# Performance work log

Hardware: AMD Instinct MI355X
Metric: run time of the kernel (lower is better)

## Reference

```python
import jax, jax.numpy as jnp
import numpy as np

B, L, C, H, W = 2, 3, 64, 32, 32
DI, N, DT_RANK, K = 128, 16, 4, 4  # d_inner=2*C, d_state, dt_rank=ceil(C/16), 4 scan dirs


def setup_inputs() -> dict:
    key = jax.random.key(0)
    ks = iter(jax.random.split(key, 48))
    nrm = lambda shape, s=0.02: jax.random.normal(next(ks), shape, jnp.float32) * s
    return {
        "image_sequence": jax.random.normal(next(ks), (B, L, C, H, W), jnp.float32),
        "difficult_zone": jax.random.normal(next(ks), (B, C, H, W), jnp.float32),
        "sigma": jax.random.uniform(next(ks), (B, C, H, W), jnp.float32),
        # LayerNorm2d applied to each frame
        "norm_g": jnp.ones((C,)), "norm_b": jnp.zeros((C,)),
        # ConvolutionalResBlock (in=3C -> out=C), GroupNorm(num_groups=1)
        "gn1_g": jnp.ones((3 * C,)), "gn1_b": jnp.zeros((3 * C,)),
        "conv1_w": nrm((C, 3 * C, 3, 3)), "conv1_b": jnp.zeros((C,)),
        "gn2_g": jnp.ones((C,)), "gn2_b": jnp.zeros((C,)),
        "conv2_w": nrm((C, C, 3, 3)), "conv2_b": jnp.zeros((C,)),
        "skip_w": nrm((C, 3 * C, 1, 1)), "skip_b": jnp.zeros((C,)),
        # VSSBlock pre-norms
        "ln1_g": jnp.ones((C,)), "ln1_b": jnp.zeros((C,)),
        "ln2_g": jnp.ones((C,)), "ln2_b": jnp.zeros((C,)),
        # SS2D
        "in_proj_w": nrm((2 * DI, C)),
        "dwconv_w": nrm((DI, 1, 3, 3)), "dwconv_b": jnp.zeros((DI,)),
        "x_proj_w": nrm((K, DT_RANK + 2 * N, DI)),
        "dt_proj_w": nrm((K, DI, DT_RANK), 0.1),
        "dt_proj_b": jnp.log(jnp.expm1(jnp.full((K, DI), 0.01, jnp.float32))),
        "A_logs": jnp.log(jnp.tile(jnp.arange(1, N + 1, dtype=jnp.float32), (K * DI, 1))),
        "Ds": jnp.ones((K * DI,)),
        "out_norm_g": jnp.ones((DI,)), "out_norm_b": jnp.zeros((DI,)),
        "out_proj_w": nrm((C, DI)),
        # Mlp (hidden = C)
        "fc1_w": nrm((C, C)), "fc1_b": jnp.zeros((C,)),
        "fc2_w": nrm((C, C)), "fc2_b": jnp.zeros((C,)),
    }


def _ln(x, g, b, eps=1e-5):  # layernorm over last axis
    m = x.mean(-1, keepdims=True)
    v = x.var(-1, keepdims=True)
    return (x - m) * jax.lax.rsqrt(v + eps) * g + b


def _ln2d(x, g, b, eps=1e-6):  # per-pixel channel layernorm, NCHW
    m = x.mean(1, keepdims=True)
    v = x.var(1, keepdims=True)
    return (x - m) * jax.lax.rsqrt(v + eps) * g[None, :, None, None] + b[None, :, None, None]


def _gn1(x, g, b, eps=1e-5):  # GroupNorm(num_groups=1), NCHW
    m = x.mean((1, 2, 3), keepdims=True)
    v = x.var((1, 2, 3), keepdims=True)
    return (x - m) * jax.lax.rsqrt(v + eps) * g[None, :, None, None] + b[None, :, None, None]


def _conv(x, w, b, pad):
    y = jax.lax.conv_general_dilated(x, w, (1, 1), [(pad, pad), (pad, pad)],
                                     dimension_numbers=("NCHW", "OIHW", "NCHW"))
    return y + b[None, :, None, None]


def _forward(image_sequence, difficult_zone, sigma, norm_g, norm_b, gn1_g, gn1_b,
             conv1_w, conv1_b, gn2_g, gn2_b, conv2_w, conv2_b, skip_w, skip_b,
             ln1_g, ln1_b, ln2_g, ln2_b, in_proj_w, dwconv_w, dwconv_b, x_proj_w,
             dt_proj_w, dt_proj_b, A_logs, Ds, out_norm_g, out_norm_b, out_proj_w,
             fc1_w, fc1_b, fc2_w, fc2_b):
    b, l, c, h, w = image_sequence.shape
    bl, L2 = b * l, h * w
    # fold frame loop into batch (identical math per frame in the torch loop)
    frames = _ln2d(image_sequence.reshape(bl, c, h, w), norm_g, norm_b)
    dz = jnp.broadcast_to(difficult_zone[:, None], (b, l, c, h, w)).reshape(bl, c, h, w)
    sg = jnp.broadcast_to(sigma[:, None], (b, l, c, h, w)).reshape(bl, c, h, w)
    x = jnp.concatenate([dz, frames, sg], axis=1)  # [bl, 3c, h, w]
    # channel compressor: pre-act conv res block
    hdn = _conv(jax.nn.silu(_gn1(x, gn1_g, gn1_b)), conv1_w, conv1_b, 1)
    hdn = _conv(jax.nn.silu(_gn1(hdn, gn2_g, gn2_b)), conv2_w, conv2_b, 1)
    x = hdn + _conv(x, skip_w, skip_b, 0)          # [bl, c, h, w]
    x = x.transpose(0, 2, 3, 1)                    # [bl, h, w, c]
    # --- VSSBlock (pre-norm): x = x + SS2D(LN(x)) ---
    xn = _ln(x, ln1_g, ln1_b)
    xz = xn @ in_proj_w.T                          # [bl,h,w,2*DI]
    xc, z = jnp.split(xz, 2, axis=-1)
    xc = xc.transpose(0, 3, 1, 2)                  # [bl, DI, h, w]
    xc = jax.lax.conv_general_dilated(xc, dwconv_w, (1, 1), [(1, 1), (1, 1)],
                                      dimension_numbers=("NCHW", "OIHW", "NCHW"),
                                      feature_group_count=DI) + dwconv_b[None, :, None, None]
    xc = jax.nn.silu(xc)
    # 4-direction scan inputs (HW, WH, and their reverses)
    xf = xc.reshape(bl, DI, L2)
    xt = xc.transpose(0, 1, 3, 2).reshape(bl, DI, L2)
    xs = jnp.stack([xf, xt], axis=1)
    xs = jnp.concatenate([xs, jnp.flip(xs, axis=-1)], axis=1)  # [bl, 4, DI, L2]
    x_dbl = jnp.einsum("bkdl,kcd->bkcl", xs, x_proj_w)
    dts, Bs, Cs = jnp.split(x_dbl, [DT_RANK, DT_RANK + N], axis=2)
    dts = jnp.einsum("bkrl,kdr->bkdl", dts, dt_proj_w) + dt_proj_b[None, :, :, None]
    dts = jax.nn.softplus(dts)                     # [bl, 4, DI, L2]
    A = -jnp.exp(A_logs).reshape(K, DI, N)
    dA = jnp.exp(dts[..., None] * A[None, :, :, None, :])            # [bl,4,DI,L2,N]
    dBu = dts[..., None] * Bs.transpose(0, 1, 3, 2)[:, :, None] * xs[..., None]
    a_t = dA.transpose(3, 0, 1, 2, 4)              # [L2, bl, 4, DI, N]
    bu_t = dBu.transpose(3, 0, 1, 2, 4)
    c_t = Cs.transpose(3, 0, 1, 2)                 # [L2, bl, 4, N]

    def step(hid, inp):
        a_i, bu_i, c_i = inp
        hid = a_i * hid + bu_i
        return hid, jnp.einsum("bkdn,bkn->bkd", hid, c_i)

    h0 = jnp.zeros((bl, K, DI, N), xs.dtype)
    _, ys = jax.lax.scan(step, h0, (a_t, bu_t, c_t))                 # [L2, bl, 4, DI]
    ys = ys.transpose(1, 2, 3, 0) + xs * Ds.reshape(K, DI)[None, :, :, None]
    inv = jnp.flip(ys[:, 2:4], axis=-1)
    y = (ys[:, 0] + inv[:, 0]
         + ys[:, 1].reshape(bl, DI, w, h).transpose(0, 1, 3, 2).reshape(bl, DI, L2)
         + inv[:, 1].reshape(bl, DI, w, h).transpose(0, 1, 3, 2).reshape(bl, DI, L2))
    y = _ln(y.transpose(0, 2, 1), out_norm_g, out_norm_b).reshape(bl, h, w, DI)
    y = y * jax.nn.silu(z)
    x = x + y @ out_proj_w.T
    # --- x = x + Mlp(LN(x)) ---
    xn = _ln(x, ln2_g, ln2_b)
    x = x + (jax.nn.gelu(xn @ fc1_w.T + fc1_b, approximate=False) @ fc2_w.T + fc2_b)
    return x.transpose(0, 3, 1, 2).reshape(b, l, c, h, w)


def reference(image_sequence, difficult_zone, sigma, norm_g, norm_b, gn1_g, gn1_b,
              conv1_w, conv1_b, gn2_g, gn2_b, conv2_w, conv2_b, skip_w, skip_b,
              ln1_g, ln1_b, ln2_g, ln2_b, in_proj_w, dwconv_w, dwconv_b, x_proj_w,
              dt_proj_w, dt_proj_b, A_logs, Ds, out_norm_g, out_norm_b, out_proj_w,
              fc1_w, fc1_b, fc2_w, fc2_b):
    return _forward(image_sequence, difficult_zone, sigma, norm_g, norm_b, gn1_g, gn1_b,
                    conv1_w, conv1_b, gn2_g, gn2_b, conv2_w, conv2_b, skip_w, skip_b,
                    ln1_g, ln1_b, ln2_g, ln2_b, in_proj_w, dwconv_w, dwconv_b, x_proj_w,
                    dt_proj_w, dt_proj_b, A_logs, Ds, out_norm_g, out_norm_b, out_proj_w,
                    fc1_w, fc1_b, fc2_w, fc2_b)
```

## Files before the change

### kernel.cpp

```cpp
#include <hip/hip_runtime.h>
#include <math.h>

#define BL    6
#define CCH   64
#define C3    192
#define L2    1024
#define DIC   128
#define NST   16
#define K4    4
#define PSTR  1088
#define NCH   32

#define LOG2E 1.44269504088896340736f
#define LN2C  0.69314718055994530942f

__device__ __forceinline__ float fexp(float x){ return __builtin_amdgcn_exp2f(x*LOG2E); }
__device__ __forceinline__ float fsilu(float x){ return x / (1.f + fexp(-x)); }
__device__ __forceinline__ float fsoftplus(float x){
  if (x > 20.f) return x;
  return __builtin_amdgcn_logf(1.f + fexp(x)) * LN2C;
}
__device__ __forceinline__ float fgelu(float x){
  return 0.5f*x*(1.f + erff(x*0.70710678118654752440f));
}

__global__ __launch_bounds__(256) void k_ln2d(const float* __restrict__ img,
    const float* __restrict__ dz, const float* __restrict__ sg,
    const float* __restrict__ g, const float* __restrict__ b, float* __restrict__ x3c,
    float* __restrict__ psum1, float* __restrict__ psq1){
  __shared__ float ps[4][16], pq[4][16], gs[4], gq[4];
  int s = blockIdx.x >> 6;
  int pg = blockIdx.x & 63;
  int tid = threadIdx.x;
  int px = tid & 15; int cg = tid >> 4;
  int wv = tid >> 6; int lane = tid & 63;
  int p = pg*16 + px;
  int bsmp = s/3;
  const float* fr = img + (size_t)s*CCH*L2;
  float vals[4]; float sm=0.f, sq=0.f;
  #pragma unroll
  for (int j=0;j<4;++j){
    int c = cg*4 + j;
    float v = fr[c*L2 + p];
    vals[j]=v; sm+=v; sq+=v*v;
  }
  sm += __shfl_xor(sm,16,64); sq += __shfl_xor(sq,16,64);
  sm += __shfl_xor(sm,32,64); sq += __shfl_xor(sq,32,64);
  if (lane < 16){ ps[wv][lane]=sm; pq[wv][lane]=sq; }
  __syncthreads();
  sm = ps[0][px]+ps[1][px]+ps[2][px]+ps[3][px];
  sq = pq[0][px]+pq[1][px]+pq[2][px]+pq[3][px];
  float mean = sm*(1.f/CCH); float var = sq*(1.f/CCH)-mean*mean;
  float rs = rsqrtf(var + 1e-6f);
  float* o = x3c + (size_t)s*C3*L2;
  const float* dzp = dz + (size_t)bsmp*CCH*L2;
  const float* sgp = sg + (size_t)bsmp*CCH*L2;
  float gsm=0.f, gsq=0.f;
  #pragma unroll
  for (int j=0;j<4;++j){
    int c = cg*4+j;
    float dzv = dzp[c*L2+p];
    float nv  = (vals[j]-mean)*rs*g[c] + b[c];
    float sgv = sgp[c*L2+p];
    o[c*L2+p] = dzv;
    o[(CCH+c)*L2+p] = nv;
    o[(2*CCH+c)*L2+p] = sgv;
    gsm += dzv+nv+sgv; gsq += dzv*dzv+nv*nv+sgv*sgv;
  }
  for (int m=1;m<64;m<<=1){ gsm+=__shfl_xor(gsm,m,64); gsq+=__shfl_xor(gsq,m,64); }
  if (lane==0){ gs[wv]=gsm; gq[wv]=gsq; }
  __syncthreads();
  if (tid==0){
    psum1[blockIdx.x] = gs[0]+gs[1]+gs[2]+gs[3];
    psq1 [blockIdx.x] = gq[0]+gq[1]+gq[2]+gq[3];
  }
}

__global__ __launch_bounds__(256) void k_gnact_pad(const float* __restrict__ x,
    const float* __restrict__ psum, const float* __restrict__ psq,
    const float* __restrict__ g, const float* __restrict__ b,
    int ch, int parts, float inv_n, float eps, float* __restrict__ out){
  int bx = blockIdx.x;
  int s = bx / ch; int c = bx % ch;
  int tid = threadIdx.x;
  float sm=0.f, sq=0.f;
  for (int i=0;i<parts;++i){ sm += psum[s*parts+i]; sq += psq[s*parts+i]; }
  float mean = sm*inv_n;
  float var = sq*inv_n - mean*mean;
  float rs = rsqrtf(var + eps);
  float gc = g[c]*rs; float bc = b[c] - mean*rs*g[c];
  float4 v = *(const float4*)(x + (size_t)bx*1024 + tid*4);
  float4 o; o.x = fsilu(v.x*gc+bc); o.y = fsilu(v.y*gc+bc);
  o.z = fsilu(v.z*gc+bc); o.w = fsilu(v.w*gc+bc);
  float* pl = out + (size_t)bx*PSTR;
  *(float4*)(pl + 32 + tid*4) = o;
  float4 z4 = make_float4(0.f,0.f,0.f,0.f);
  if (tid < 8)  *(float4*)(pl + tid*4) = z4;
  else if (tid < 16) *(float4*)(pl + 1056 + (tid-8)*4) = z4;
}

__device__ __forceinline__ void conv_row_acc(float4& a0, float4& a1, float4 mid, float lf, float rt,
    const float* wp0, const float* wp1){
  float w0=wp0[0], w1=wp0[1], w2=wp0[2];
  a0.x = fmaf(w0,lf,   fmaf(w1,mid.x, fmaf(w2,mid.y, a0.x)));
  a0.y = fmaf(w0,mid.x,fmaf(w1,mid.y, fmaf(w2,mid.z, a0.y)));
  a0.z = fmaf(w0,mid.y,fmaf(w1,mid.z, fmaf(w2,mid.w, a0.z)));
  a0.w = fmaf(w0,mid.z,fmaf(w1,mid.w, fmaf(w2,rt,    a0.w)));
  float v0=wp1[0], v1=wp1[1], v2=wp1[2];
  a1.x = fmaf(v0,lf,   fmaf(v1,mid.x, fmaf(v2,mid.y, a1.x)));
  a1.y = fmaf(v0,mid.x,fmaf(v1,mid.y, fmaf(v2,mid.z, a1.y)));
  a1.z = fmaf(v0,mid.y,fmaf(v1,mid.z, fmaf(v2,mid.w, a1.z)));
  a1.w = fmaf(v0,mid.z,fmaf(v1,mid.w, fmaf(v2,rt,    a1.w)));
}

__device__ __forceinline__ void conv_ci_body(float4 m0, float4 m1, float4 m2, int q,
    const float* wp0, const float* wp1, float4& a0, float4& a1){
  float lf0=__shfl_up(m0.w,1,64), rt0=__shfl_down(m0.x,1,64);
  float lf1=__shfl_up(m1.w,1,64), rt1=__shfl_down(m1.x,1,64);
  float lf2=__shfl_up(m2.w,1,64), rt2=__shfl_down(m2.x,1,64);
  if (q==0){ lf0=0.f; lf1=0.f; lf2=0.f; }
  if (q==7){ rt0=0.f; rt1=0.f; rt2=0.f; }
  conv_row_acc(a0,a1,m0,lf0,rt0, wp0+0, wp1+0);
  conv_row_acc(a0,a1,m1,lf1,rt1, wp0+3, wp1+3);
  conv_row_acc(a0,a1,m2,lf2,rt2, wp0+6, wp1+6);
}

__global__ __launch_bounds__(256) void k_conv1_split(const float* __restrict__ xact,
    const float* __restrict__ w, float* __restrict__ part){
  int bx = blockIdx.x; int kk = bx&7; int cop=(bx>>3)&31; int s=bx>>8;
  int co0 = cop*2, co1 = co0+1;
  int tid = threadIdx.x; int row = tid>>3; int q = tid&7; int col0 = q*4;
  float4 a0 = make_float4(0.f,0.f,0.f,0.f);
  float4 a1 = make_float4(0.f,0.f,0.f,0.f);
  int ci0 = kk*24;
  const float* pl = xact + ((size_t)s*C3 + ci0)*PSTR + row*32 + col0;
  const float* wp0 = w + (size_t)(co0*C3 + ci0)*9;
  const float* wp1 = w + (size_t)(co1*C3 + ci0)*9;
  float4 m0 = *(const float4*)(pl);
  float4 m1 = *(const float4*)(pl+32);
  float4 m2 = *(const float4*)(pl+64);
  #pragma unroll 2
  for (int i=0;i<24;++i){
    const float* pn = pl + (i<23 ? PSTR : 0);
    float4 n0 = *(const float4*)(pn);
    float4 n1 = *(const float4*)(pn+32);
    float4 n2 = *(const float4*)(pn+64);
    conv_ci_body(m0,m1,m2,q, wp0, wp1, a0, a1);
    wp0 += 9; wp1 += 9; pl = pn; m0=n0; m1=n1; m2=n2;
  }
  float* pp = part + (size_t)kk*(BL*CCH*L2) + ((size_t)s*CCH+co0)*L2 + row*32+col0;
  *(float4*)pp = a0;
  *(float4*)(pp+L2) = a1;
}

__global__ __launch_bounds__(256) void k_reduce1(const float* __restrict__ part,
    const float* __restrict__ bias, float* __restrict__ h1,
    float* __restrict__ psum2, float* __restrict__ psq2){
  int co = blockIdx.x & 63; int s = blockIdx.x >> 6;
  size_t ofs = ((size_t)s*CCH+co)*L2 + threadIdx.x*4;
  const size_t stride = (size_t)BL*CCH*L2;
  float4 acc = *(const float4*)(part + ofs);
  #pragma unroll
  for (int kk=1;kk<8;++kk){
    float4 r = *(const float4*)(part + (size_t)kk*stride + ofs);
    acc.x += r.x; acc.y += r.y; acc.z += r.z; acc.w += r.w;
  }
  float bv = bias[co];
  acc.x += bv; acc.y += bv; acc.z += bv; acc.w += bv;
  *(float4*)(h1 + ofs) = acc;
  float sm = acc.x+acc.y+acc.z+acc.w;
  float sq = acc.x*acc.x+acc.y*acc.y+acc.z*acc.z+acc.w*acc.w;
  for (int m=1;m<64;m<<=1){ sm+=__shfl_xor(sm,m,64); sq+=__shfl_xor(sq,m,64); }
  __shared__ float s_sm[4], s_sq[4];
  int wv = threadIdx.x>>6;
  if ((threadIdx.x&63)==0){ s_sm[wv]=sm; s_sq[wv]=sq; }
  __syncthreads();
  if (threadIdx.x==0){
    psum2[blockIdx.x] = s_sm[0]+s_sm[1]+s_sm[2]+s_sm[3];
    psq2 [blockIdx.x] = s_sq[0]+s_sq[1]+s_sq[2]+s_sq[3];
  }
}

__global__ __launch_bounds__(256) void k_conv2_split(const float* __restrict__ xact2,
    const float* __restrict__ x3c, const float* __restrict__ w2,
    const float* __restrict__ wsk, float* __restrict__ part){
  int t = blockIdx.x; int role = t % 3; t /= 3;
  int cop = t & 31; int s = t >> 5;
  int co0 = cop*2, co1 = co0+1;
  int tid = threadIdx.x; int row = tid>>3; int q = tid&7; int col0 = q*4;
  int p = row*32+col0;
  float4 a0 = make_float4(0.f,0.f,0.f,0.f);
  float4 a1 = make_float4(0.f,0.f,0.f,0.f);
  if (role < 2){
    int ci0 = role*32;
    const float* pl = xact2 + ((size_t)s*CCH + ci0)*PSTR + row*32 + col0;
    const float* wp0 = w2 + (size_t)(co0*CCH + ci0)*9;
    const float* wp1 = w2 + (size_t)(co1*CCH + ci0)*9;
    float4 m0 = *(const float4*)(pl);
    float4 m1 = *(const float4*)(pl+32);
    float4 m2 = *(const float4*)(pl+64);
    #pragma unroll 2
    for (int i=0;i<32;++i){
      const float* pn = pl + (i<31 ? PSTR : 0);
      float4 n0 = *(const float4*)(pn);
      float4 n1 = *(const float4*)(pn+32);
      float4 n2 = *(const float4*)(pn+64);
      conv_ci_body(m0,m1,m2,q, wp0, wp1, a0, a1);
      wp0 += 9; wp1 += 9; pl = pn; m0=n0; m1=n1; m2=n2;
    }
  } else {
    const float* x3 = x3c + (size_t)s*C3*L2 + p;
    #pragma unroll 4
    for (int ci=0; ci<C3; ++ci){
      float4 v = *(const float4*)(x3 + (size_t)ci*L2);
      float ws0 = wsk[co0*C3+ci], ws1 = wsk[co1*C3+ci];
      a0.x = fmaf(ws0,v.x,a0.x); a0.y = fmaf(ws0,v.y,a0.y); a0.z = fmaf(ws0,v.z,a0.z); a0.w = fmaf(ws0,v.w,a0.w);
      a1.x = fmaf(ws1,v.x,a1.x); a1.y = fmaf(ws1,v.y,a1.y); a1.z = fmaf(ws1,v.z,a1.z); a1.w = fmaf(ws1,v.w,a1.w);
    }
  }
  float* pp = part + (size_t)role*(BL*CCH*L2) + ((size_t)s*CCH+co0)*L2 + p;
  *(float4*)pp = a0;
  *(float4*)(pp+L2) = a1;
}

__global__ __launch_bounds__(256) void k_reduce2(const float* __restrict__ part,
    const float* __restrict__ b2, const float* __restrict__ bsk,
    float* __restrict__ xp, float* __restrict__ x_cmaj){
  int co = blockIdx.x & 63; int s = blockIdx.x >> 6;
  int p = threadIdx.x*4;
  size_t ofs = ((size_t)s*CCH+co)*L2 + p;
  const size_t stride = (size_t)BL*CCH*L2;
  float4 r0 = *(const float4*)(part + ofs);
  float4 r1 = *(const float4*)(part + stride + ofs);
  float4 r2 = *(const float4*)(part + 2*stride + ofs);
  float bv = b2[co]+bsk[co];
  float4 o;
  o.x = r0.x+r1.x+r2.x+bv;
  o.y = r0.y+r1.y+r2.y+bv;
  o.z = r0.z+r1.z+r2.z+bv;
  o.w = r0.w+r1.w+r2.w+bv;
  *(float4*)(x_cmaj + ofs) = o;
  float* xpb = xp + ((size_t)s*L2 + p)*CCH + co;
  xpb[0] = o.x; xpb[CCH] = o.y; xpb[2*CCH] = o.z; xpb[3*CCH] = o.w;
}

__global__ __launch_bounds__(256) void k_ln1_inproj(const float* __restrict__ xp,
    const float* __restrict__ g, const float* __restrict__ b, const float* __restrict__ W,
    float* __restrict__ xc, float* __restrict__ z_t){
  __shared__ float xn_s[64*65];
  int bx = blockIdx.x; int oq = bx & 3; int pg = (bx>>2)&15; int s = bx>>6;
  int p0 = pg*64;
  int tid = threadIdx.x; int wv = __builtin_amdgcn_readfirstlane(tid>>6); int lane = tid&63;
  for (int j=0;j<16;++j){
    int pl = wv*16 + j; int p = p0 + pl;
    float v = xp[((size_t)s*L2 + p)*CCH + lane];
    float sm = v, sq = v*v;
    for (int m=1;m<64;m<<=1){ sm += __shfl_xor(sm,m,64); sq += __shfl_xor(sq,m,64); }
    float mean = sm*(1.f/64.f); float var = sq*(1.f/64.f) - mean*mean;
    float rs = rsqrtf(var + 1e-5f);
    xn_s[pl*65 + lane] = (v-mean)*rs*g[lane] + b[lane];
  }
  __syncthreads();
  int px_l = tid & 63;
  int og = __builtin_amdgcn_readfirstlane(tid >> 6);
  int o0 = oq*64 + og*16;
  float acc[16];
  #pragma unroll
  for (int oi=0;oi<16;++oi) acc[oi]=0.f;
  for (int c=0;c<64;++c){
    float xv = xn_s[px_l*65 + c];
    #pragma unroll
    for (int oi=0;oi<16;++oi) acc[oi] = fmaf(W[(o0+oi)*64 + c], xv, acc[oi]);
  }
  int p = p0 + px_l;
  if (oq < 2){
    #pragma unroll
    for (int oi=0;oi<16;++oi) xc[((size_t)s*DIC + o0 + oi)*L2 + p] = acc[oi];
  } else {
    #pragma unroll
    for (int oi=0;oi<16;++oi) z_t[((size_t)s*DIC + (o0-128) + oi)*L2 + p] = acc[oi];
  }
}

__global__ __launch_bounds__(256) void k_dwconv(const float* __restrict__ xc,
    const float* __restrict__ w, const float* __restrict__ bias, float* __restrict__ xconv){
  int bx = blockIdx.x; int dch = bx & 127; int s = bx >> 7;
  int tid = threadIdx.x; int row = tid>>3; int q = tid&7; int col0 = q*4;
  const float* xr = xc + ((size_t)s*DIC+dch)*L2;
  const float* wp = w + dch*9;
  float bv = bias[dch];
  float4 acc = make_float4(bv,bv,bv,bv);
  #pragma unroll
  for (int dy=-1;dy<=1;++dy){
    int r = row+dy;
    float4 mid = make_float4(0.f,0.f,0.f,0.f);
    if (0<=r && r<32) mid = *(const float4*)(xr + r*32 + col0);
    float lf = __shfl_up(mid.w,1,64); if(q==0) lf=0.f;
    float rt = __shfl_down(mid.x,1,64); if(q==7) rt=0.f;
    float w0=wp[(dy+1)*3], w1=wp[(dy+1)*3+1], w2=wp[(dy+1)*3+2];
    acc.x = fmaf(w0,lf,   fmaf(w1,mid.x, fmaf(w2,mid.y, acc.x)));
    acc.y = fmaf(w0,mid.x,fmaf(w1,mid.y, fmaf(w2,mid.z, acc.y)));
    acc.z = fmaf(w0,mid.y,fmaf(w1,mid.z, fmaf(w2,mid.w, acc.z)));
    acc.w = fmaf(w0,mid.z,fmaf(w1,mid.w, fmaf(w2,rt,    acc.w)));
  }
  acc.x = fsilu(acc.x); acc.y = fsilu(acc.y); acc.z = fsilu(acc.z); acc.w = fsilu(acc.w);
  *(float4*)(xconv + ((size_t)s*DIC+dch)*L2 + row*32+col0) = acc;
}

__global__ __launch_bounds__(256) void k_xproj_dt(const float* __restrict__ xconv,
    const float* __restrict__ W,
    float* __restrict__ dtr, float* __restrict__ Bp, float* __restrict__ Cp,
    float* __restrict__ u_t){
  __shared__ float smem[128*68];
  int bx = blockIdx.x; int pg = bx & 15; int sk = bx >> 4;
  int k = sk & 3; int s = sk >> 2;
  int tid = threadIdx.x;
  for (int i = tid; i < 128*16; i += 256){
    int dr = i>>4; int j4 = (i&15)*4;
    float4 v = *(const float4*)(xconv + ((size_t)(s*DIC + dr))*L2 + pg*64 + j4);
    *(float4*)&smem[dr*68 + j4] = v;
  }
  __syncthreads();
  if (k == 0){
    float* ub = u_t + ((size_t)(s*L2) + pg*64)*DIC;
    for (int i = tid; i < 64*128; i += 256){
      int px2 = i>>7; int dd = i&127;
      ub[(size_t)px2*DIC + dd] = smem[dd*68 + px2];
    }
  }
  int px = tid & 63;
  int cgrp = __builtin_amdgcn_readfirstlane(tid >> 6);
  int c0 = cgrp*9;
  const float* wb = W + (size_t)(k*36 + c0)*DIC;
  float acc[9];
  #pragma unroll
  for (int ci=0;ci<9;++ci) acc[ci]=0.f;
  for (int d=0; d<DIC; ++d){
    float xv = smem[d*68 + px];
    #pragma unroll
    for (int ci=0;ci<9;++ci) acc[ci] = fmaf(wb[ci*DIC+d], xv, acc[ci]);
  }
  __syncthreads();
  #pragma unroll
  for (int ci=0;ci<9;++ci) smem[(c0+ci)*68 + px] = acc[ci];
  __syncthreads();
  {
    int pp = tid >> 2; int r = tid & 3;
    dtr[((size_t)sk*L2 + pg*64 + pp)*4 + r] = smem[r*68 + pp];
  }
  float* Bb = Bp + ((size_t)sk*L2 + pg*64)*NST;
  float* Cb = Cp + ((size_t)sk*L2 + pg*64)*NST;
  for (int i = tid; i < 1024; i += 256){
    int pp = i>>4; int n = i&15;
    Bb[pp*NST + n] = smem[(4+n)*68 + pp];
    Cb[pp*NST + n] = smem[(20+n)*68 + pp];
  }
}

__device__ __forceinline__ int scan_pix32(int ch, int j, int k){
  if (k==0) return ch*32 + j;
  if (k==1) return j*32 + ch;
  if (k==2) return 1023 - (ch*32 + j);
  return 1023 - (j*32 + ch);
}

struct StepB { float4 dt4; float uv; float4 B0,B1,B2,B3; };
__device__ __forceinline__ StepB loadB(const float* dr, const float* ub, const float* Bb, int p){
  StepB r;
  r.dt4 = *(const float4*)(dr + (size_t)p*4);
  r.uv = ub[(size_t)p*DIC];
  const float* bp = Bb + p*NST;
  r.B0 = *(const float4*)bp; r.B1 = *(const float4*)(bp+4);
  r.B2 = *(const float4*)(bp+8); r.B3 = *(const float4*)(bp+12);
  return r;
}
__device__ __forceinline__ float dt_eval(float4 w4, float bb, float4 d4){
  return fsoftplus(fmaf(w4.x,d4.x,fmaf(w4.y,d4.y,fmaf(w4.z,d4.z,fmaf(w4.w,d4.w,bb)))));
}

__global__ __launch_bounds__(256,2) void k_scan_part3(const float* __restrict__ dtr,
    const float* __restrict__ dtw, const float* __restrict__ dtb,
    const float* __restrict__ u_t, const float* __restrict__ Bp,
    const float* __restrict__ A_logs, float* __restrict__ hend, float* __restrict__ Ssum){
  int bx = blockIdx.x; int chp = bx & 15; int sk = bx >> 4;
  int k = sk & 3; int s = sk >> 2;
  int tid = threadIdx.x; int d = tid & 127; int ch = chp*2 + (tid>>7);
  float aco[16];
  {
    const float* ab = A_logs + (size_t)(k*DIC+d)*NST;
    #pragma unroll
    for (int n=0;n<16;++n) aco[n] = -LOG2E * fexp(ab[n]);
  }
  float4 w4 = *(const float4*)(dtw + (size_t)(k*DIC+d)*4);
  float bb = dtb[k*DIC+d];
  float h[16]; float Sacc = 0.f;
  #pragma unroll
  for (int n=0;n<16;++n) h[n]=0.f;
  const float* dr = dtr + (size_t)sk*L2*4;
  const float* ub = u_t + (size_t)s*L2*DIC + d;
  const float* Bb = Bp + (size_t)sk*L2*NST;
  StepB cur = loadB(dr, ub, Bb, scan_pix32(ch, 0, k));
  #pragma unroll 4
  for (int j=0;j<32;++j){
    StepB nxt;
    if (j < 31) nxt = loadB(dr, ub, Bb, scan_pix32(ch, j+1, k));
    float dtv = dt_eval(w4, bb, cur.dt4);
    Sacc += dtv;
    float tv = dtv*cur.uv;
    #define PSTEP(NI, BV) { float a_ = __builtin_amdgcn_exp2f(dtv*aco[NI]); \
      h[NI] = fmaf(a_, h[NI], tv*(BV)); }
    PSTEP(0,cur.B0.x) PSTEP(1,cur.B0.y) PSTEP(2,cur.B0.z) PSTEP(3,cur.B0.w)
    PSTEP(4,cur.B1.x) PSTEP(5,cur.B1.y) PSTEP(6,cur.B1.z) PSTEP(7,cur.B1.w)
    PSTEP(8,cur.B2.x) PSTEP(9,cur.B2.y) PSTEP(10,cur.B2.z) PSTEP(11,cur.B2.w)
    PSTEP(12,cur.B3.x) PSTEP(13,cur.B3.y) PSTEP(14,cur.B3.z) PSTEP(15,cur.B3.w)
    #undef PSTEP
    cur = nxt;
  }
  size_t base = ((size_t)(sk*NCH + ch)*DIC + d)*NST;
  #pragma unroll
  for (int q4=0;q4<4;++q4)
    *(float4*)(hend + base + q4*4)  = make_float4(h[q4*4],h[q4*4+1],h[q4*4+2],h[q4*4+3]);
  Ssum[(size_t)(sk*NCH + ch)*DIC + d] = Sacc;
}

__global__ __launch_bounds__(256) void k_scan_fix3(const float* __restrict__ hend,
    const float* __restrict__ Ssum, const float* __restrict__ A_logs,
    float* __restrict__ Hin){
  int t = blockIdx.x*256 + threadIdx.x;
  int n = t & 15; int d = (t>>4) & 127; int sk = t >> 11; int k = sk & 3;
  float aco = -LOG2E * fexp(A_logs[(size_t)(k*DIC+d)*NST + n]);
  float H = 0.f;
  #pragma unroll 8
  for (int ch=0; ch<NCH; ++ch){
    size_t sidx = (size_t)(sk*NCH + ch)*DIC + d;
    float pa = __builtin_amdgcn_exp2f(aco * Ssum[sidx]);
    float he = hend[sidx*NST + n];
    Hin[sidx*NST + n] = H;
    H = fmaf(pa, H, he);
  }
}

__global__ __launch_bounds__(256,2) void k_scan_y3(const float* __restrict__ dtr,
    const float* __restrict__ dtw, const float* __restrict__ dtb,
    const float* __restrict__ u_t, const float* __restrict__ Bp, const float* __restrict__ Cp,
    const float* __restrict__ A_logs, const float* __restrict__ Ds,
    const float* __restrict__ Hin, float* __restrict__ ys_t){
  int bx = blockIdx.x; int chp = bx & 15; int sk = bx >> 4;
  int k = sk & 3; int s = sk >> 2;
  int tid = threadIdx.x; int d = tid & 127; int ch = chp*2 + (tid>>7);
  float aco[16];
  {
    const float* ab = A_logs + (size_t)(k*DIC+d)*NST;
    #pragma unroll
    for (int n=0;n<16;++n) aco[n] = -LOG2E * fexp(ab[n]);
  }
  float4 w4 = *(const float4*)(dtw + (size_t)(k*DIC+d)*4);
  float bb = dtb[k*DIC+d];
  float Dv = Ds[k*DIC+d];
  float h[16];
  size_t hbase = ((size_t)(sk*NCH + ch)*DIC + d)*NST;
  #pragma unroll
  for (int q4=0;q4<4;++q4){
    float4 hv = *(const float4*)(Hin + hbase + q4*4);
    h[q4*4]=hv.x; h[q4*4+1]=hv.y; h[q4*4+2]=hv.z; h[q4*4+3]=hv.w;
  }
  const float* dr = dtr + (size_t)sk*L2*4;
  const float* ub = u_t + (size_t)s*L2*DIC + d;
  const float* Bb = Bp + (size_t)sk*L2*NST;
  const float* Cb = Cp + (size_t)sk*L2*NST;
  float* yb = ys_t + (size_t)sk*L2*DIC + d;
  int pcur = scan_pix32(ch, 0, k);
  StepB cur = loadB(dr, ub, Bb, pcur);
  float4 Cc0 = *(const float4*)(Cb + pcur*NST);
  float4 Cc1 = *(const float4*)(Cb + pcur*NST + 4);
  float4 Cc2 = *(const float4*)(Cb + pcur*NST + 8);
  float4 Cc3 = *(const float4*)(Cb + pcur*NST + 12);
  #pragma unroll 4
  for (int j=0;j<32;++j){
    StepB nxt; float4 Cn0, Cn1, Cn2, Cn3; int pn = pcur;
    if (j < 31){
      pn = scan_pix32(ch, j+1, k);
      nxt = loadB(dr, ub, Bb, pn);
      Cn0 = *(const float4*)(Cb + pn*NST);
      Cn1 = *(const float4*)(Cb + pn*NST + 4);
      Cn2 = *(const float4*)(Cb + pn*NST + 8);
      Cn3 = *(const float4*)(Cb + pn*NST + 12);
    }
    float dtv = dt_eval(w4, bb, cur.dt4);
    float tv = dtv*cur.uv;
    float y0=0.f, y1=0.f, y2=0.f, y3=0.f;
    #define YSTEP(NI, BV, CV, YA) { float a_ = __builtin_amdgcn_exp2f(dtv*aco[NI]); \
      h[NI] = fmaf(a_, h[NI], tv*(BV)); YA = fmaf(h[NI], (CV), YA); }
    YSTEP(0,cur.B0.x,Cc0.x,y0) YSTEP(1,cur.B0.y,Cc0.y,y1) YSTEP(2,cur.B0.z,Cc0.z,y2) YSTEP(3,cur.B0.w,Cc0.w,y3)
    YSTEP(4,cur.B1.x,Cc1.x,y0) YSTEP(5,cur.B1.y,Cc1.y,y1) YSTEP(6,cur.B1.z,Cc1.z,y2) YSTEP(7,cur.B1.w,Cc1.w,y3)
    YSTEP(8,cur.B2.x,Cc2.x,y0) YSTEP(9,cur.B2.y,Cc2.y,y1) YSTEP(10,cur.B2.z,Cc2.z,y2) YSTEP(11,cur.B2.w,Cc2.w,y3)
    YSTEP(12,cur.B3.x,Cc3.x,y0) YSTEP(13,cur.B3.y,Cc3.y,y1) YSTEP(14,cur.B3.z,Cc3.z,y2) YSTEP(15,cur.B3.w,Cc3.w,y3)
    #undef YSTEP
    yb[(size_t)pcur*DIC] = fmaf(cur.uv, Dv, (y0+y1)+(y2+y3));
    cur = nxt; Cc0 = Cn0; Cc1 = Cn1; Cc2 = Cn2; Cc3 = Cn3; pcur = pn;
  }
}

__global__ __launch_bounds__(256) void k_tail(const float* __restrict__ ys_t,
    const float* __restrict__ z_t, const float* __restrict__ ong, const float* __restrict__ onb,
    const float* __restrict__ Wop, const float* __restrict__ x_cmaj,
    const float* __restrict__ g2, const float* __restrict__ b2n,
    const float* __restrict__ w1, const float* __restrict__ b1,
    const float* __restrict__ w2, const float* __restrict__ b2,
    float* __restrict__ out){
  __shared__ float yt[128*17];
  __shared__ float xvt[64*17];
  __shared__ float ts[64*17];
  int s = blockIdx.x >> 6; int pg = blockIdx.x & 63;
  int tid = threadIdx.x;
  {
    int wv = __builtin_amdgcn_readfirstlane(tid>>6); int lane = tid&63;
    int d0 = lane, d1 = lane+64;
    for (int i=0;i<4;++i){
      int px = i*4 + wv; int p = pg*16 + px;
      const float* yb = ys_t + ((size_t)(s*4)*L2 + p)*DIC;
      float ya = yb[d0] + yb[(size_t)L2*DIC + d0] + yb[(size_t)2*L2*DIC + d0] + yb[(size_t)3*L2*DIC + d0];
      float yc = yb[d1] + yb[(size_t)L2*DIC + d1] + yb[(size_t)2*L2*DIC + d1] + yb[(size_t)3*L2*DIC + d1];
      float sm = ya+yc, sq = ya*ya+yc*yc;
      for (int m=1;m<64;m<<=1){ sm+=__shfl_xor(sm,m,64); sq+=__shfl_xor(sq,m,64); }
      float mean = sm*(1.f/128.f); float var = sq*(1.f/128.f)-mean*mean;
      float rs = rsqrtf(var + 1e-5f);
      float yn0 = (ya-mean)*rs*ong[d0] + onb[d0];
      float yn1 = (yc-mean)*rs*ong[d1] + onb[d1];
      float zv0 = z_t[((size_t)s*DIC+d0)*L2 + p];
      float zv1 = z_t[((size_t)s*DIC+d1)*L2 + p];
      yt[d0*17 + px] = yn0 * fsilu(zv0);
      yt[d1*17 + px] = yn1 * fsilu(zv1);
    }
  }
  __syncthreads();
  {
    int px = tid & 15; int cgp = tid >> 4;
    int c0 = cgp*4;
    float a0=0.f,a1=0.f,a2=0.f,a3=0.f;
    for (int d=0; d<DIC; ++d){
      float yv = yt[d*17 + px];
      a0 = fmaf(Wop[(c0+0)*DIC + d], yv, a0);
      a1 = fmaf(Wop[(c0+1)*DIC + d], yv, a1);
      a2 = fmaf(Wop[(c0+2)*DIC + d], yv, a2);
      a3 = fmaf(Wop[(c0+3)*DIC + d], yv, a3);
    }
    int p = pg*16 + px;
    size_t base = ((size_t)s*CCH + c0)*L2 + p;
    xvt[(c0+0)*17 + px] = x_cmaj[base]      + a0;
    xvt[(c0+1)*17 + px] = x_cmaj[base+L2]   + a1;
    xvt[(c0+2)*17 + px] = x_cmaj[base+2*L2] + a2;
    xvt[(c0+3)*17 + px] = x_cmaj[base+3*L2] + a3;
  }
  __syncthreads();
  int px = tid & 15; int cgp = tid >> 4;
  float sm=0.f, sq=0.f;
  for (int c=0;c<64;++c){ float v = xvt[c*17+px]; sm+=v; sq+=v*v; }
  float mean = sm*(1.f/64.f);
  float rs = rsqrtf(sq*(1.f/64.f) - mean*mean + 1e-5f);
  int o0 = cgp*4;
  float t[4];
  #pragma unroll
  for (int oi=0;oi<4;++oi) t[oi] = b1[o0+oi];
  for (int c=0;c<64;++c){
    float xn = (xvt[c*17+px]-mean)*rs*g2[c] + b2n[c];
    #pragma unroll
    for (int oi=0;oi<4;++oi) t[oi] = fmaf(xn, w1[(o0+oi)*64 + c], t[oi]);
  }
  #pragma unroll
  for (int oi=0;oi<4;++oi) ts[(o0+oi)*17 + px] = fgelu(t[oi]);
  __syncthreads();
  int c0 = cgp*4;
  float acc[4];
  #pragma unroll
  for (int ci=0;ci<4;++ci) acc[ci] = xvt[(c0+ci)*17+px] + b2[c0+ci];
  for (int o=0;o<64;++o){
    float tv = ts[o*17+px];
    #pragma unroll
    for (int ci=0;ci<4;++ci) acc[ci] = fmaf(tv, w2[(c0+ci)*64 + o], acc[ci]);
  }
  int p = pg*16 + px;
  #pragma unroll
  for (int ci=0;ci<4;++ci) out[((size_t)s*CCH + c0+ci)*L2 + p] = acc[ci];
}

extern "C" void kernel_launch(void* const* d_in, const int* in_sizes, int n_in,
                              void* d_out, int out_size, void* d_ws, size_t ws_size,
                              hipStream_t stream){
  (void)in_sizes; (void)n_in; (void)out_size; (void)ws_size;
  const float* img      = (const float*)d_in[0];
  const float* dz       = (const float*)d_in[1];
  const float* sg       = (const float*)d_in[2];
  const float* norm_g   = (const float*)d_in[3];
  const float* norm_b   = (const float*)d_in[4];
  const float* gn1_g    = (const float*)d_in[5];
  const float* gn1_b    = (const float*)d_in[6];
  const float* conv1_w  = (const float*)d_in[7];
  const float* conv1_b  = (const float*)d_in[8];
  const float* gn2_g    = (const float*)d_in[9];
  const float* gn2_b    = (const float*)d_in[10];
  const float* conv2_w  = (const float*)d_in[11];
  const float* conv2_b  = (const float*)d_in[12];
  const float* skip_w   = (const float*)d_in[13];
  const float* skip_b   = (const float*)d_in[14];
  const float* ln1_g    = (const float*)d_in[15];
  const float* ln1_b    = (const float*)d_in[16];
  const float* ln2_g    = (const float*)d_in[17];
  const float* ln2_b    = (const float*)d_in[18];
  const float* in_proj_w= (const float*)d_in[19];
  const float* dwconv_w = (const float*)d_in[20];
  const float* dwconv_b = (const float*)d_in[21];
  const float* x_proj_w = (const float*)d_in[22];
  const float* dt_proj_w= (const float*)d_in[23];
  const float* dt_proj_b= (const float*)d_in[24];
  const float* A_logs   = (const float*)d_in[25];
  const float* Ds       = (const float*)d_in[26];
  const float* out_norm_g = (const float*)d_in[27];
  const float* out_norm_b = (const float*)d_in[28];
  const float* out_proj_w = (const float*)d_in[29];
  const float* fc1_w    = (const float*)d_in[30];
  const float* fc1_b    = (const float*)d_in[31];
  const float* fc2_w    = (const float*)d_in[32];
  const float* fc2_b    = (const float*)d_in[33];

  float* ws = (float*)d_ws;
  float* x3c    = ws;
  float* xact1  = x3c    + 1179648;
  float* h1     = xact1  + 1253376;
  float* xact2  = h1     + 393216;
  float* xp     = xact2  + 417792;
  float* x_cmaj = xp     + 393216;
  float* z_t    = x_cmaj + 393216;
  float* xc     = z_t    + 786432;
  float* xconv  = xc     + 786432;
  float* hole   = xconv  + 786432;
  float* scanbuf= hole   + 884736;
  float* ys_t   = scanbuf+ 3145728;
  float* statsb = ys_t   + 3145728;
  float* psum1  = statsb;
  float* psq1   = statsb + 384;
  float* psum2  = statsb + 768;
  float* psq2   = statsb + 1152;
  float* part1  = scanbuf;
  float* part2  = ys_t;
  float* hend   = x3c;
  float* u_t    = h1;
  float* Bp     = xp;
  float* Cp     = xc;
  float* dtr    = hole;
  float* Ssum   = hole + 98304;
  float* Hin    = scanbuf;

  k_ln2d<<<384, 256, 0, stream>>>(img, dz, sg, norm_g, norm_b, x3c, psum1, psq1);
  k_gnact_pad<<<6*C3, 256, 0, stream>>>(x3c, psum1, psq1, gn1_g, gn1_b, C3, 64,
                                        1.f/(C3*L2), 1e-5f, xact1);
  k_conv1_split<<<1536, 256, 0, stream>>>(xact1, conv1_w, part1);
  k_reduce1<<<384, 256, 0, stream>>>(part1, conv1_b, h1, psum2, psq2);
  k_gnact_pad<<<6*CCH, 256, 0, stream>>>(h1, psum2, psq2, gn2_g, gn2_b, CCH, 64,
                                         1.f/(CCH*L2), 1e-5f, xact2);
  k_conv2_split<<<576, 256, 0, stream>>>(xact2, x3c, conv2_w, skip_w, part2);
  k_reduce2<<<384, 256, 0, stream>>>(part2, conv2_b, skip_b, xp, x_cmaj);
  k_ln1_inproj<<<384, 256, 0, stream>>>(xp, ln1_g, ln1_b, in_proj_w, xc, z_t);
  k_dwconv<<<768, 256, 0, stream>>>(xc, dwconv_w, dwconv_b, xconv);
  k_xproj_dt<<<384, 256, 0, stream>>>(xconv, x_proj_w, dtr, Bp, Cp, u_t);
  k_scan_part3<<<384, 256, 0, stream>>>(dtr, dt_proj_w, dt_proj_b, u_t, Bp, A_logs, hend, Ssum);
  k_scan_fix3<<<192, 256, 0, stream>>>(hend, Ssum, A_logs, Hin);
  k_scan_y3<<<384, 256, 0, stream>>>(dtr, dt_proj_w, dt_proj_b, u_t, Bp, Cp, A_logs, Ds, Hin, ys_t);
  k_tail<<<384, 256, 0, stream>>>(ys_t, z_t, out_norm_g, out_norm_b, out_proj_w, x_cmaj,
                                  ln2_g, ln2_b, fc1_w, fc1_b, fc2_w, fc2_b, (float*)d_out);
}
```

Measured before the change: 304.7 us.

## Fuse skip conv into LN kernel, dwconv into xproj, widen conv output tiles

Moves the 1x1 skip projection into the LN2d kernel, which already holds the 192-channel pixel tile, and writes it to a separate buffer as a third partial for reduce2. The depthwise conv+SiLU is fused into the x_proj staging loop, which removes one kernel launch and the round trip of the xconv intermediate through global memory. conv1 and conv2 now compute 8 and 4 output channels per block instead of 2, so each input load is reused across more FMAs, at the cost of fewer blocks (384 and 192) and more registers.

```diff
diff --git a/kernel.cpp b/kernel.cpp
--- a/kernel.cpp
+++ b/kernel.cpp
@@ -26,8 +26,11 @@
 
 __global__ __launch_bounds__(256) void k_ln2d(const float* __restrict__ img,
     const float* __restrict__ dz, const float* __restrict__ sg,
-    const float* __restrict__ g, const float* __restrict__ b, float* __restrict__ x3c,
+    const float* __restrict__ g, const float* __restrict__ b,
+    const float* __restrict__ wsk,
+    float* __restrict__ x3c, float* __restrict__ skipb,
     float* __restrict__ psum1, float* __restrict__ psq1){
+  __shared__ float xt[192*17];
   __shared__ float ps[4][16], pq[4][16], gs[4], gq[4];
   int s = blockIdx.x >> 6;
   int pg = blockIdx.x & 63;
@@ -65,6 +68,9 @@
     o[c*L2+p] = dzv;
     o[(CCH+c)*L2+p] = nv;
     o[(2*CCH+c)*L2+p] = sgv;
+    xt[c*17 + px] = dzv;
+    xt[(CCH+c)*17 + px] = nv;
+    xt[(2*CCH+c)*17 + px] = sgv;
     gsm += dzv+nv+sgv; gsq += dzv*dzv+nv*nv+sgv*sgv;
   }
   for (int m=1;m<64;m<<=1){ gsm+=__shfl_xor(gsm,m,64); gsq+=__shfl_xor(gsq,m,64); }
@@ -74,6 +80,25 @@
     psum1[blockIdx.x] = gs[0]+gs[1]+gs[2]+gs[3];
     psq1 [blockIdx.x] = gq[0]+gq[1]+gq[2]+gq[3];
   }
+  int cog = tid >> 4;
+  float a0=0.f,a1=0.f,a2=0.f,a3=0.f;
+  const float* w0p = wsk + (size_t)(cog*4+0)*C3;
+  const float* w1p = wsk + (size_t)(cog*4+1)*C3;
+  const float* w2p = wsk + (size_t)(cog*4+2)*C3;
+  const float* w3p = wsk + (size_t)(cog*4+3)*C3;
+  #pragma unroll 4
+  for (int ci=0; ci<C3; ++ci){
+    float xv = xt[ci*17 + px];
+    a0 = fmaf(w0p[ci], xv, a0);
+    a1 = fmaf(w1p[ci], xv, a1);
+    a2 = fmaf(w2p[ci], xv, a2);
+    a3 = fmaf(w3p[ci], xv, a3);
+  }
+  size_t sb = ((size_t)s*CCH + cog*4)*L2 + p;
+  skipb[sb]        = a0;
+  skipb[sb + L2]   = a1;
+  skipb[sb + 2*L2] = a2;
+  skipb[sb + 3*L2] = a3;
 }
 
 __global__ __launch_bounds__(256) void k_gnact_pad(const float* __restrict__ x,
@@ -99,58 +124,62 @@
   else if (tid < 16) *(float4*)(pl + 1056 + (tid-8)*4) = z4;
 }
 
-__device__ __forceinline__ void conv_row_acc(float4& a0, float4& a1, float4 mid, float lf, float rt,
-    const float* wp0, const float* wp1){
-  float w0=wp0[0], w1=wp0[1], w2=wp0[2];
-  a0.x = fmaf(w0,lf,   fmaf(w1,mid.x, fmaf(w2,mid.y, a0.x)));
-  a0.y = fmaf(w0,mid.x,fmaf(w1,mid.y, fmaf(w2,mid.z, a0.y)));
-  a0.z = fmaf(w0,mid.y,fmaf(w1,mid.z, fmaf(w2,mid.w, a0.z)));
-  a0.w = fmaf(w0,mid.z,fmaf(w1,mid.w, fmaf(w2,rt,    a0.w)));
-  float v0=wp1[0], v1=wp1[1], v2=wp1[2];
-  a1.x = fmaf(v0,lf,   fmaf(v1,mid.x, fmaf(v2,mid.y, a1.x)));
-  a1.y = fmaf(v0,mid.x,fmaf(v1,mid.y, fmaf(v2,mid.z, a1.y)));
-  a1.z = fmaf(v0,mid.y,fmaf(v1,mid.z, fmaf(v2,mid.w, a1.z)));
-  a1.w = fmaf(v0,mid.z,fmaf(v1,mid.w, fmaf(v2,rt,    a1.w)));
-}
-
-__device__ __forceinline__ void conv_ci_body(float4 m0, float4 m1, float4 m2, int q,
-    const float* wp0, const float* wp1, float4& a0, float4& a1){
+template<int NCO>
+__device__ __forceinline__ void conv_ci_accN(float4 m0, float4 m1, float4 m2, int q,
+    const float* __restrict__ wbase, int coStride9, float4* a){
   float lf0=__shfl_up(m0.w,1,64), rt0=__shfl_down(m0.x,1,64);
   float lf1=__shfl_up(m1.w,1,64), rt1=__shfl_down(m1.x,1,64);
   float lf2=__shfl_up(m2.w,1,64), rt2=__shfl_down(m2.x,1,64);
   if (q==0){ lf0=0.f; lf1=0.f; lf2=0.f; }
   if (q==7){ rt0=0.f; rt1=0.f; rt2=0.f; }
-  conv_row_acc(a0,a1,m0,lf0,rt0, wp0+0, wp1+0);
-  conv_row_acc(a0,a1,m1,lf1,rt1, wp0+3, wp1+3);
-  conv_row_acc(a0,a1,m2,lf2,rt2, wp0+6, wp1+6);
+  #pragma unroll
+  for (int co=0; co<NCO; ++co){
+    const float* wp = wbase + co*coStride9;
+    float4& A = a[co];
+    float w0=wp[0], w1=wp[1], w2=wp[2];
+    A.x = fmaf(w0,lf0,   fmaf(w1,m0.x, fmaf(w2,m0.y, A.x)));
+    A.y = fmaf(w0,m0.x,  fmaf(w1,m0.y, fmaf(w2,m0.z, A.y)));
+    A.z = fmaf(w0,m0.y,  fmaf(w1,m0.z, fmaf(w2,m0.w, A.z)));
+    A.w = fmaf(w0,m0.z,  fmaf(w1,m0.w, fmaf(w2,rt0,  A.w)));
+    float v0=wp[3], v1=wp[4], v2=wp[5];
+    A.x = fmaf(v0,lf1,   fmaf(v1,m1.x, fmaf(v2,m1.y, A.x)));
+    A.y = fmaf(v0,m1.x,  fmaf(v1,m1.y, fmaf(v2,m1.z, A.y)));
+    A.z = fmaf(v0,m1.y,  fmaf(v1,m1.z, fmaf(v2,m1.w, A.z)));
+    A.w = fmaf(v0,m1.z,  fmaf(v1,m1.w, fmaf(v2,rt1,  A.w)));
+    float u0=wp[6], u1=wp[7], u2=wp[8];
+    A.x = fmaf(u0,lf2,   fmaf(u1,m2.x, fmaf(u2,m2.y, A.x)));
+    A.y = fmaf(u0,m2.x,  fmaf(u1,m2.y, fmaf(u2,m2.z, A.y)));
+    A.z = fmaf(u0,m2.y,  fmaf(u1,m2.z, fmaf(u2,m2.w, A.z)));
+    A.w = fmaf(u0,m2.z,  fmaf(u1,m2.w, fmaf(u2,rt2,  A.w)));
+  }
 }
 
 __global__ __launch_bounds__(256) void k_conv1_split(const float* __restrict__ xact,
     const float* __restrict__ w, float* __restrict__ part){
-  int bx = blockIdx.x; int kk = bx&7; int cop=(bx>>3)&31; int s=bx>>8;
-  int co0 = cop*2, co1 = co0+1;
+  int bx = blockIdx.x; int kk = bx&7; int cog=(bx>>3)&7; int s=bx>>6;
+  int co0 = cog*8;
   int tid = threadIdx.x; int row = tid>>3; int q = tid&7; int col0 = q*4;
-  float4 a0 = make_float4(0.f,0.f,0.f,0.f);
-  float4 a1 = make_float4(0.f,0.f,0.f,0.f);
+  float4 a[8];
+  #pragma unroll
+  for (int co=0;co<8;++co) a[co] = make_float4(0.f,0.f,0.f,0.f);
   int ci0 = kk*24;
   const float* pl = xact + ((size_t)s*C3 + ci0)*PSTR + row*32 + col0;
-  const float* wp0 = w + (size_t)(co0*C3 + ci0)*9;
-  const float* wp1 = w + (size_t)(co1*C3 + ci0)*9;
+  const float* wb = w + (size_t)(co0*C3 + ci0)*9;
+  const int coStride9 = C3*9;
   float4 m0 = *(const float4*)(pl);
   float4 m1 = *(const float4*)(pl+32);
   float4 m2 = *(const float4*)(pl+64);
-  #pragma unroll 2
   for (int i=0;i<24;++i){
     const float* pn = pl + (i<23 ? PSTR : 0);
     float4 n0 = *(const float4*)(pn);
     float4 n1 = *(const float4*)(pn+32);
     float4 n2 = *(const float4*)(pn+64);
-    conv_ci_body(m0,m1,m2,q, wp0, wp1, a0, a1);
-    wp0 += 9; wp1 += 9; pl = pn; m0=n0; m1=n1; m2=n2;
+    conv_ci_accN<8>(m0,m1,m2,q, wb, coStride9, a);
+    wb += 9; pl = pn; m0=n0; m1=n1; m2=n2;
   }
   float* pp = part + (size_t)kk*(BL*CCH*L2) + ((size_t)s*CCH+co0)*L2 + row*32+col0;
-  *(float4*)pp = a0;
-  *(float4*)(pp+L2) = a1;
+  #pragma unroll
+  for (int co=0;co<8;++co) *(float4*)(pp + (size_t)co*L2) = a[co];
 }
 
 __global__ __launch_bounds__(256) void k_reduce1(const float* __restrict__ part,
@@ -182,45 +211,32 @@
 }
 
 __global__ __launch_bounds__(256) void k_conv2_split(const float* __restrict__ xact2,
-    const float* __restrict__ x3c, const float* __restrict__ w2,
-    const float* __restrict__ wsk, float* __restrict__ part){
-  int t = blockIdx.x; int role = t % 3; t /= 3;
-  int cop = t & 31; int s = t >> 5;
-  int co0 = cop*2, co1 = co0+1;
+    const float* __restrict__ w2, float* __restrict__ part){
+  int bx = blockIdx.x; int role = bx & 1; int cog = (bx>>1) & 15; int s = bx >> 5;
+  int co0 = cog*4;
   int tid = threadIdx.x; int row = tid>>3; int q = tid&7; int col0 = q*4;
   int p = row*32+col0;
-  float4 a0 = make_float4(0.f,0.f,0.f,0.f);
-  float4 a1 = make_float4(0.f,0.f,0.f,0.f);
-  if (role < 2){
-    int ci0 = role*32;
-    const float* pl = xact2 + ((size_t)s*CCH + ci0)*PSTR + row*32 + col0;
-    const float* wp0 = w2 + (size_t)(co0*CCH + ci0)*9;
-    const float* wp1 = w2 + (size_t)(co1*CCH + ci0)*9;
-    float4 m0 = *(const float4*)(pl);
-    float4 m1 = *(const float4*)(pl+32);
-    float4 m2 = *(const float4*)(pl+64);
-    #pragma unroll 2
-    for (int i=0;i<32;++i){
-      const float* pn = pl + (i<31 ? PSTR : 0);
-      float4 n0 = *(const float4*)(pn);
-      float4 n1 = *(const float4*)(pn+32);
-      float4 n2 = *(const float4*)(pn+64);
-      conv_ci_body(m0,m1,m2,q, wp0, wp1, a0, a1);
-      wp0 += 9; wp1 += 9; pl = pn; m0=n0; m1=n1; m2=n2;
-    }
-  } else {
-    const float* x3 = x3c + (size_t)s*C3*L2 + p;
-    #pragma unroll 4
-    for (int ci=0; ci<C3; ++ci){
-      float4 v = *(const float4*)(x3 + (size_t)ci*L2);
-      float ws0 = wsk[co0*C3+ci], ws1 = wsk[co1*C3+ci];
-      a0.x = fmaf(ws0,v.x,a0.x); a0.y = fmaf(ws0,v.y,a0.y); a0.z = fmaf(ws0,v.z,a0.z); a0.w = fmaf(ws0,v.w,a0.w);
-      a1.x = fmaf(ws1,v.x,a1.x); a1.y = fmaf(ws1,v.y,a1.y); a1.z = fmaf(ws1,v.z,a1.z); a1.w = fmaf(ws1,v.w,a1.w);
-    }
+  float4 a[4];
+  #pragma unroll
+  for (int co=0;co<4;++co) a[co] = make_float4(0.f,0.f,0.f,0.f);
+  int ci0 = role*32;
+  const float* pl = xact2 + ((size_t)s*CCH + ci0)*PSTR + row*32 + col0;
+  const float* wb = w2 + (size_t)(co0*CCH + ci0)*9;
+  const int coStride9 = CCH*9;
+  float4 m0 = *(const float4*)(pl);
+  float4 m1 = *(const float4*)(pl+32);
+  float4 m2 = *(const float4*)(pl+64);
+  for (int i=0;i<32;++i){
+    const float* pn = pl + (i<31 ? PSTR : 0);
+    float4 n0 = *(const float4*)(pn);
+    float4 n1 = *(const float4*)(pn+32);
+    float4 n2 = *(const float4*)(pn+64);
+    conv_ci_accN<4>(m0,m1,m2,q, wb, coStride9, a);
+    wb += 9; pl = pn; m0=n0; m1=n1; m2=n2;
   }
   float* pp = part + (size_t)role*(BL*CCH*L2) + ((size_t)s*CCH+co0)*L2 + p;
-  *(float4*)pp = a0;
-  *(float4*)(pp+L2) = a1;
+  #pragma unroll
+  for (int co=0;co<4;++co) *(float4*)(pp + (size_t)co*L2) = a[co];
 }
 
 __global__ __launch_bounds__(256) void k_reduce2(const float* __restrict__ part,
@@ -282,32 +298,8 @@
   }
 }
 
-__global__ __launch_bounds__(256) void k_dwconv(const float* __restrict__ xc,
-    const float* __restrict__ w, const float* __restrict__ bias, float* __restrict__ xconv){
-  int bx = blockIdx.x; int dch = bx & 127; int s = bx >> 7;
-  int tid = threadIdx.x; int row = tid>>3; int q = tid&7; int col0 = q*4;
-  const float* xr = xc + ((size_t)s*DIC+dch)*L2;
-  const float* wp = w + dch*9;
-  float bv = bias[dch];
-  float4 acc = make_float4(bv,bv,bv,bv);
-  #pragma unroll
-  for (int dy=-1;dy<=1;++dy){
-    int r = row+dy;
-    float4 mid = make_float4(0.f,0.f,0.f,0.f);
-    if (0<=r && r<32) mid = *(const float4*)(xr + r*32 + col0);
-    float lf = __shfl_up(mid.w,1,64); if(q==0) lf=0.f;
-    float rt = __shfl_down(mid.x,1,64); if(q==7) rt=0.f;
-    float w0=wp[(dy+1)*3], w1=wp[(dy+1)*3+1], w2=wp[(dy+1)*3+2];
-    acc.x = fmaf(w0,lf,   fmaf(w1,mid.x, fmaf(w2,mid.y, acc.x)));
-    acc.y = fmaf(w0,mid.x,fmaf(w1,mid.y, fmaf(w2,mid.z, acc.y)));
-    acc.z = fmaf(w0,mid.y,fmaf(w1,mid.z, fmaf(w2,mid.w, acc.z)));
-    acc.w = fmaf(w0,mid.z,fmaf(w1,mid.w, fmaf(w2,rt,    acc.w)));
-  }
-  acc.x = fsilu(acc.x); acc.y = fsilu(acc.y); acc.z = fsilu(acc.z); acc.w = fsilu(acc.w);
-  *(float4*)(xconv + ((size_t)s*DIC+dch)*L2 + row*32+col0) = acc;
-}
-
-__global__ __launch_bounds__(256) void k_xproj_dt(const float* __restrict__ xconv,
+__global__ __launch_bounds__(256) void k_xproj_dt(const float* __restrict__ xc,
+    const float* __restrict__ dww, const float* __restrict__ dwb,
     const float* __restrict__ W,
     float* __restrict__ dtr, float* __restrict__ Bp, float* __restrict__ Cp,
     float* __restrict__ u_t){
@@ -317,8 +309,28 @@
   int tid = threadIdx.x;
   for (int i = tid; i < 128*16; i += 256){
     int dr = i>>4; int j4 = (i&15)*4;
-    float4 v = *(const float4*)(xconv + ((size_t)(s*DIC + dr))*L2 + pg*64 + j4);
-    *(float4*)&smem[dr*68 + j4] = v;
+    int rw = j4>>5; int col0 = j4 & 31;
+    int gr = pg*2 + rw;
+    int q = i&7;
+    const float* xr = xc + ((size_t)s*DIC+dr)*L2;
+    const float* wp = dww + dr*9;
+    float bv = dwb[dr];
+    float4 acc = make_float4(bv,bv,bv,bv);
+    #pragma unroll
+    for (int dy=-1;dy<=1;++dy){
+      int r = gr+dy;
+      float4 mid = make_float4(0.f,0.f,0.f,0.f);
+      if (0<=r && r<32) mid = *(const float4*)(xr + r*32 + col0);
+      float lf = __shfl_up(mid.w,1,64); if(q==0) lf=0.f;
+      float rt = __shfl_down(mid.x,1,64); if(q==7) rt=0.f;
+      float w0=wp[(dy+1)*3], w1=wp[(dy+1)*3+1], w2=wp[(dy+1)*3+2];
+      acc.x = fmaf(w0,lf,   fmaf(w1,mid.x, fmaf(w2,mid.y, acc.x)));
+      acc.y = fmaf(w0,mid.x,fmaf(w1,mid.y, fmaf(w2,mid.z, acc.y)));
+      acc.z = fmaf(w0,mid.y,fmaf(w1,mid.z, fmaf(w2,mid.w, acc.z)));
+      acc.w = fmaf(w0,mid.z,fmaf(w1,mid.w, fmaf(w2,rt,    acc.w)));
+    }
+    acc.x = fsilu(acc.x); acc.y = fsilu(acc.y); acc.z = fsilu(acc.z); acc.w = fsilu(acc.w);
+    *(float4*)&smem[dr*68 + j4] = acc;
   }
   __syncthreads();
   if (k == 0){
@@ -643,6 +655,7 @@
   float* psq2   = statsb + 1152;
   float* part1  = scanbuf;
   float* part2  = ys_t;
+  float* skipb  = part2 + 2*(size_t)(BL*CCH*L2);
   float* hend   = x3c;
   float* u_t    = h1;
   float* Bp     = xp;
@@ -651,18 +664,17 @@
   float* Ssum   = hole + 98304;
   float* Hin    = scanbuf;
 
-  k_ln2d<<<384, 256, 0, stream>>>(img, dz, sg, norm_g, norm_b, x3c, psum1, psq1);
+  k_ln2d<<<384, 256, 0, stream>>>(img, dz, sg, norm_g, norm_b, skip_w, x3c, skipb, psum1, psq1);
   k_gnact_pad<<<6*C3, 256, 0, stream>>>(x3c, psum1, psq1, gn1_g, gn1_b, C3, 64,
                                         1.f/(C3*L2), 1e-5f, xact1);
-  k_conv1_split<<<1536, 256, 0, stream>>>(xact1, conv1_w, part1);
+  k_conv1_split<<<384, 256, 0, stream>>>(xact1, conv1_w, part1);
   k_reduce1<<<384, 256, 0, stream>>>(part1, conv1_b, h1, psum2, psq2);
   k_gnact_pad<<<6*CCH, 256, 0, stream>>>(h1, psum2, psq2, gn2_g, gn2_b, CCH, 64,
                                          1.f/(CCH*L2), 1e-5f, xact2);
-  k_conv2_split<<<576, 256, 0, stream>>>(xact2, x3c, conv2_w, skip_w, part2);
+  k_conv2_split<<<192, 256, 0, stream>>>(xact2, conv2_w, part2);
   k_reduce2<<<384, 256, 0, stream>>>(part2, conv2_b, skip_b, xp, x_cmaj);
   k_ln1_inproj<<<384, 256, 0, stream>>>(xp, ln1_g, ln1_b, in_proj_w, xc, z_t);
-  k_dwconv<<<768, 256, 0, stream>>>(xc, dwconv_w, dwconv_b, xconv);
-  k_xproj_dt<<<384, 256, 0, stream>>>(xconv, x_proj_w, dtr, Bp, Cp, u_t);
+  k_xproj_dt<<<384, 256, 0, stream>>>(xc, dwconv_w, dwconv_b, x_proj_w, dtr, Bp, Cp, u_t);
   k_scan_part3<<<384, 256, 0, stream>>>(dtr, dt_proj_w, dt_proj_b, u_t, Bp, A_logs, hend, Ssum);
   k_scan_fix3<<<192, 256, 0, stream>>>(hend, Ssum, A_logs, Hin);
   k_scan_y3<<<384, 256, 0, stream>>>(dtr, dt_proj_w, dt_proj_b, u_t, Bp, Cp, A_logs, Ds, Hin, ys_t);
```

Result: slower. 323.9 us (+6.3%).
